# Kernel tuning notes

Measured on AMD Instinct MI355X. Metric: run time of the kernel, lower is better.

The kernel has to match this reference:

```python
import jax, jax.numpy as jnp
import numpy as np

N_NODES = 50000
N_EDGES = 800000
D = 128  # d_feat == hidden_channels


def setup_inputs() -> dict:
    key = jax.random.key(0)
    ks = jax.random.split(key, 7)
    s = 1.0 / np.sqrt(D)
    return {
        "x": jax.random.normal(ks[0], (N_NODES, D), dtype=jnp.float32),
        "edge_index": jax.random.randint(ks[1], (2, N_EDGES), 0, N_NODES, dtype=jnp.int64),
        "W1_l": jax.random.normal(ks[2], (D, D), dtype=jnp.float32) * s,
        "b1": jnp.zeros((D,), dtype=jnp.float32),
        "W1_r": jax.random.normal(ks[3], (D, D), dtype=jnp.float32) * s,
        "W2_l": jax.random.normal(ks[4], (D, D), dtype=jnp.float32) * s,
        "b2": jnp.zeros((D,), dtype=jnp.float32),
        "W2_r": jax.random.normal(ks[5], (D, D), dtype=jnp.float32) * s,
    }


def reference(x, edge_index, W1_l, b1, W1_r, W2_l, b2, W2_r):
    src = edge_index[0]
    dst = edge_index[1]
    n = x.shape[0]
    # in-degree for mean aggregation (zero-degree nodes get 0 aggregate)
    deg = jax.ops.segment_sum(jnp.ones_like(src, dtype=x.dtype), dst, num_segments=n)
    inv_deg = (1.0 / jnp.maximum(deg, 1.0))[:, None]  # [N,1]

    def sage_conv(h, Wl, b, Wr):
        # mean over incoming neighbor messages, then lin_l(agg) + lin_r(h)
        agg = jax.ops.segment_sum(h[src], dst, num_segments=n) * inv_deg  # [N,D]
        return agg @ Wl + b + h @ Wr

    h = jax.nn.relu(sage_conv(x, W1_l, b1, W1_r))
    return sage_conv(h, W2_l, b2, W2_r)
```

## Files before the change

### kernel.cpp

```cpp
#include <hip/hip_runtime.h>
#include <hip/hip_bf16.h>

typedef __attribute__((ext_vector_type(8))) short bf16x8;
typedef __attribute__((ext_vector_type(4))) float f32x4;

#define CAP 64

static __device__ inline unsigned short f2b(float f) {
    unsigned u = __float_as_uint(f);
    unsigned r = (u + 0x7FFFu + ((u >> 16) & 1u)) >> 16;
    return (unsigned short)r;
}
static __device__ inline float blo(unsigned u) { return __uint_as_float(u << 16); }
static __device__ inline float bhi(unsigned u) { return __uint_as_float(u & 0xFFFF0000u); }

__global__ void zero_kernel(int* __restrict__ p, int n) {
    int i = blockIdx.x * blockDim.x + threadIdx.x;
    if (i < n) p[i] = 0;
}

__global__ void fill_kernel(const int* __restrict__ ei, int* __restrict__ cursor,
                            unsigned short* __restrict__ edge16, int E, int N) {
    int e = blockIdx.x * blockDim.x + threadIdx.x;
    if (e >= E) return;
    int s = ei[e];
    int d = ei[E + e];
    if ((unsigned)d >= (unsigned)N) return;
    if ((unsigned)s >= (unsigned)N) s = 0;
    int pos = atomicAdd(&cursor[d], 1);
    if (pos < CAP) edge16[(size_t)d * CAP + pos] = (unsigned short)s;
}

__global__ __launch_bounds__(256) void x2b_kernel(const float* __restrict__ x,
                                                  unsigned short* __restrict__ xb,
                                                  int n4) {
    int i = blockIdx.x * blockDim.x + threadIdx.x;
    if (i >= n4) return;
    float4 v = ((const float4*)x)[i];
    ushort4 b;
    b.x = f2b(v.x); b.y = f2b(v.y); b.z = f2b(v.z); b.w = f2b(v.w);
    ((ushort4*)xb)[i] = b;
}

__global__ __launch_bounds__(256) void aggregate_kernel(
        const unsigned short* __restrict__ in, const int* __restrict__ cursor,
        const unsigned short* __restrict__ edge16, const int* __restrict__ ei,
        unsigned short* __restrict__ agg, int E, int N) {
    int node = blockIdx.x * 4 + (threadIdx.x >> 6);
    if (node >= N) return;
    int lane = threadIdx.x & 63;
    int g = lane >> 4;
    int f = lane & 15;
    int deg = cursor[node];

    float acc[8];
    #pragma unroll
    for (int i = 0; i < 8; ++i) acc[i] = 0.f;

    if (deg <= CAP) {
        const unsigned short* base = edge16 + (size_t)node * CAP;
        int idx = (lane < deg) ? (int)base[lane] : 0;
        #pragma unroll 4
        for (int j = 0; j < deg; j += 4) {
            int e = j + g;
            int s = __shfl(idx, e & 63);
            if (e < deg) {
                uint4 v = *(const uint4*)(in + (size_t)s * 128 + f * 8);
                acc[0] += blo(v.x); acc[1] += bhi(v.x);
                acc[2] += blo(v.y); acc[3] += bhi(v.y);
                acc[4] += blo(v.z); acc[5] += bhi(v.z);
                acc[6] += blo(v.w); acc[7] += bhi(v.w);
            }
        }
    } else {
        for (int j = 0; j < E; j += 4) {
            int e = j + g;
            bool act = (e < E) && (ei[E + e] == node);
            if (act) {
                int s = ei[e];
                if ((unsigned)s >= (unsigned)N) s = 0;
                uint4 v = *(const uint4*)(in + (size_t)s * 128 + f * 8);
                acc[0] += blo(v.x); acc[1] += bhi(v.x);
                acc[2] += blo(v.y); acc[3] += bhi(v.y);
                acc[4] += blo(v.z); acc[5] += bhi(v.z);
                acc[6] += blo(v.w); acc[7] += bhi(v.w);
            }
        }
    }

    #pragma unroll
    for (int d = 16; d <= 32; d <<= 1) {
        #pragma unroll
        for (int i = 0; i < 8; ++i) acc[i] += __shfl_xor(acc[i], d);
    }

    if (g == 0) {
        float inv = 1.0f / (float)(deg > 1 ? deg : 1);
        uint4 o;
        o.x = (unsigned)f2b(acc[0] * inv) | ((unsigned)f2b(acc[1] * inv) << 16);
        o.y = (unsigned)f2b(acc[2] * inv) | ((unsigned)f2b(acc[3] * inv) << 16);
        o.z = (unsigned)f2b(acc[4] * inv) | ((unsigned)f2b(acc[5] * inv) << 16);
        o.w = (unsigned)f2b(acc[6] * inv) | ((unsigned)f2b(acc[7] * inv) << 16);
        *(uint4*)(agg + (size_t)node * 128 + f * 8) = o;
    }
}

__global__ void prep_w_kernel(const float* __restrict__ W1l, const float* __restrict__ W1r,
                              const float* __restrict__ W2l, const float* __restrict__ W2r,
                              unsigned short* __restrict__ wt) {
    int n = blockIdx.x & 127;
    int layer = blockIdx.x >> 7;
    int k = threadIdx.x;
    const float* Wlp = layer ? W2l : W1l;
    const float* Wrp = layer ? W2r : W1r;
    unsigned short* dst = wt + (size_t)layer * 128 * 256 + (size_t)n * 256;
    dst[k]       = f2b(Wlp[(size_t)k * 128 + n]);
    dst[k + 128] = f2b(Wrp[(size_t)k * 128 + n]);
}

template<int RELU, int OUT_BF16>
__global__ __launch_bounds__(256) void gemm_mfma_kernel(
        const unsigned short* __restrict__ Arow, const unsigned short* __restrict__ Xrow,
        const unsigned short* __restrict__ Wt, const float* __restrict__ bias,
        void* __restrict__ outp, int n) {
    constexpr int LDK = 264;
    __shared__ unsigned short sA[64 * LDK];
    int tid = threadIdx.x;
    int row0 = blockIdx.x * 64;

    #pragma unroll
    for (int it = 0; it < 8; ++it) {
        int c = tid + it * 256;
        int r = c >> 5;
        int q = c & 31;
        int row = row0 + r; if (row >= n) row = n - 1;
        uint4 v = (q < 16) ? ((const uint4*)(Arow + (size_t)row * 128))[q]
                           : ((const uint4*)(Xrow + (size_t)row * 128))[q - 16];
        *(uint4*)&sA[r * LDK + q * 8] = v;
    }
    __syncthreads();

    int lane = tid & 63;
    int wave = tid >> 6;
    int quad = lane >> 4;
    int tm   = lane & 15;

    f32x4 acc[4][2];
    #pragma unroll
    for (int m = 0; m < 4; ++m)
        #pragma unroll
        for (int j = 0; j < 2; ++j)
            acc[m][j] = (f32x4){0.f, 0.f, 0.f, 0.f};

    const unsigned short* wb0 = Wt + (size_t)(wave * 32 + tm) * 256;

    #pragma unroll
    for (int ks = 0; ks < 8; ++ks) {
        int k0 = ks * 32 + quad * 8;
        bf16x8 a[4], b[2];
        #pragma unroll
        for (int m = 0; m < 4; ++m)
            a[m] = *(const bf16x8*)&sA[(m * 16 + tm) * LDK + k0];
        #pragma unroll
        for (int j = 0; j < 2; ++j)
            b[j] = *(const bf16x8*)(wb0 + (size_t)j * 16 * 256 + k0);
        #pragma unroll
        for (int m = 0; m < 4; ++m)
            #pragma unroll
            for (int j = 0; j < 2; ++j)
                acc[m][j] = __builtin_amdgcn_mfma_f32_16x16x32_bf16(a[m], b[j], acc[m][j], 0, 0, 0);
    }

    #pragma unroll
    for (int j = 0; j < 2; ++j) {
        int ncol = wave * 32 + j * 16 + tm;
        float bb = bias[ncol];
        #pragma unroll
        for (int m = 0; m < 4; ++m) {
            #pragma unroll
            for (int reg = 0; reg < 4; ++reg) {
                int row = row0 + m * 16 + quad * 4 + reg;
                if (row >= n) continue;
                float v = acc[m][j][reg] + bb;
                if (RELU) v = v > 0.f ? v : 0.f;
                if (OUT_BF16)
                    ((unsigned short*)outp)[(size_t)row * 128 + ncol] = f2b(v);
                else
                    ((float*)outp)[(size_t)row * 128 + ncol] = v;
            }
        }
    }
}

extern "C" void kernel_launch(void* const* d_in, const int* in_sizes, int n_in,
                              void* d_out, int out_size, void* d_ws, size_t ws_size,
                              hipStream_t stream) {
    const float* x   = (const float*)d_in[0];
    const int*   ei  = (const int*)d_in[1];
    const float* W1l = (const float*)d_in[2];
    const float* b1  = (const float*)d_in[3];
    const float* W1r = (const float*)d_in[4];
    const float* W2l = (const float*)d_in[5];
    const float* b2  = (const float*)d_in[6];
    const float* W2r = (const float*)d_in[7];
    float* out = (float*)d_out;

    const int D = 128;
    const int N = in_sizes[0] / D;
    const int E = in_sizes[1] / 2;

    char* ws = (char*)d_ws;
    size_t off = 0;
    auto alloc = [&](size_t bytes) {
        size_t o = off;
        off = (off + bytes + 511) & ~(size_t)511;
        return (void*)(ws + o);
    };
    int*            cursor  = (int*)           alloc((size_t)N * 4);
    unsigned short* edge16  = (unsigned short*)alloc((size_t)N * CAP * 2);
    unsigned short* agg_bf  = (unsigned short*)alloc((size_t)N * D * 2);
    unsigned short* xb      = (unsigned short*)alloc((size_t)N * D * 2);
    unsigned short* wt      = (unsigned short*)alloc((size_t)2 * 128 * 256 * 2);
    unsigned short* h_bf = xb;
    (void)ws_size; (void)n_in; (void)out_size;

    zero_kernel<<<(N + 255) / 256, 256, 0, stream>>>(cursor, N);
    fill_kernel<<<(E + 255) / 256, 256, 0, stream>>>(ei, cursor, edge16, E, N);

    int n4 = N * D / 4;
    x2b_kernel<<<(n4 + 255) / 256, 256, 0, stream>>>(x, xb, n4);
    prep_w_kernel<<<256, 128, 0, stream>>>(W1l, W1r, W2l, W2r, wt);
    const unsigned short* wt1 = wt;
    const unsigned short* wt2 = wt + (size_t)128 * 256;

    int agg_grid  = (N + 3) / 4;
    int gemm_grid = (N + 63) / 64;

    aggregate_kernel<<<agg_grid, 256, 0, stream>>>(xb, cursor, edge16, ei, agg_bf, E, N);
    gemm_mfma_kernel<1, 1><<<gemm_grid, 256, 0, stream>>>(agg_bf, xb, wt1, b1, (void*)h_bf, N);

    aggregate_kernel<<<agg_grid, 256, 0, stream>>>(h_bf, cursor, edge16, ei, agg_bf, E, N);
    gemm_mfma_kernel<0, 0><<<gemm_grid, 256, 0, stream>>>(agg_bf, h_bf, wt2, b2, (void*)out, N);
}
```

Measured before the change: 239.0 us.

## Shard edge-bucket fill by destination range across XCD-interleaved blocks

Replaces the one-thread-per-edge fill kernel with a sharded version. Each of 8 shards of blocks handles only the edges whose destination falls in one contiguous node range, and consecutive block IDs map to different shards. The intent is to keep the atomics and scattered writes for a given node range inside one chiplet's L2 (blocks are round-robined across XCDs), reducing cross-die cache traffic. The cost is that every edge's destination is read 8 times and 7/8 of the loads are discarded.

```diff
diff --git a/kernel.cpp b/kernel.cpp
--- a/kernel.cpp
+++ b/kernel.cpp
@@ -5,6 +5,7 @@
 typedef __attribute__((ext_vector_type(4))) float f32x4;
 
 #define CAP 64
+#define SH  8
 
 static __device__ inline unsigned short f2b(float f) {
     unsigned u = __float_as_uint(f);
@@ -19,16 +20,24 @@
     if (i < n) p[i] = 0;
 }
 
-__global__ void fill_kernel(const int* __restrict__ ei, int* __restrict__ cursor,
-                            unsigned short* __restrict__ edge16, int E, int N) {
-    int e = blockIdx.x * blockDim.x + threadIdx.x;
-    if (e >= E) return;
-    int s = ei[e];
-    int d = ei[E + e];
-    if ((unsigned)d >= (unsigned)N) return;
-    if ((unsigned)s >= (unsigned)N) s = 0;
-    int pos = atomicAdd(&cursor[d], 1);
-    if (pos < CAP) edge16[(size_t)d * CAP + pos] = (unsigned short)s;
+__global__ __launch_bounds__(256) void fill_shard_kernel(
+        const int* __restrict__ ei, int* __restrict__ cursor,
+        unsigned short* __restrict__ edge16, int E, int N, int G, int npg) {
+    int s = blockIdx.x & (SH - 1);
+    int i = blockIdx.x >> 3;
+    int d_lo = s * npg;
+    int d_hi = d_lo + npg; if (d_hi > N) d_hi = N;
+    int C = (E + G - 1) / G;
+    int e0 = i * C;
+    int e1 = e0 + C; if (e1 > E) e1 = E;
+    for (int e = e0 + threadIdx.x; e < e1; e += 256) {
+        int d = ei[E + e];
+        if (d < d_lo || d >= d_hi) continue;
+        int src = ei[e];
+        if ((unsigned)src >= (unsigned)N) src = 0;
+        int pos = atomicAdd(&cursor[d], 1);
+        if (pos < CAP) edge16[(size_t)d * CAP + pos] = (unsigned short)src;
+    }
 }
 
 __global__ __launch_bounds__(256) void x2b_kernel(const float* __restrict__ x,
@@ -225,7 +234,11 @@
     (void)ws_size; (void)n_in; (void)out_size;
 
     zero_kernel<<<(N + 255) / 256, 256, 0, stream>>>(cursor, N);
-    fill_kernel<<<(E + 255) / 256, 256, 0, stream>>>(ei, cursor, edge16, E, N);
+    {
+        int G = 256;
+        int npg = (N + SH - 1) / SH;
+        fill_shard_kernel<<<SH * G, 256, 0, stream>>>(ei, cursor, edge16, E, N, G, npg);
+    }
 
     int n4 = N * D / 4;
     x2b_kernel<<<(n4 + 255) / 256, 256, 0, stream>>>(x, xb, n4);
```

Measured after the change: 229.8 us. -3.9%, faster.
